# Kernel tuning notes

Hardware: AMD Instinct MI355X
Metric: run time of the kernel (lower is better)

Reference implementation:

```python
import jax, jax.numpy as jnp
import numpy as np

NEG_SLOPE = 0.2
BN_EPS = 1e-5
SM_EPS = 1e-16


def gatv2_conv(x, src, dst, num_nodes, Wl, bl, Wr, br, att, bias, concat):
    # x: [N, Fin]; att: [H, C]
    H, C = att.shape
    xl = (x @ Wl + bl).reshape(-1, H, C)  # source-side (x_j), lin_l
    xr = (x @ Wr + br).reshape(-1, H, C)  # target-side (x_i), lin_r
    e = jax.nn.leaky_relu(xl[src] + xr[dst], NEG_SLOPE)          # [E, H, C]
    logits = jnp.einsum('ehc,hc->eh', e, att)                    # [E, H]
    m = jax.ops.segment_max(logits, dst, num_segments=num_nodes)  # [N, H]
    expv = jnp.exp(logits - m[dst])
    denom = jax.ops.segment_sum(expv, dst, num_segments=num_nodes)
    alpha = expv / (denom[dst] + SM_EPS)                          # [E, H]
    msg = xl[src] * alpha[:, :, None]                             # [E, H, C]
    out = jax.ops.segment_sum(msg, dst, num_segments=num_nodes)   # [N, H, C]
    out = out.reshape(num_nodes, H * C) if concat else out.mean(axis=1)
    return out + bias


def batchnorm(x, gamma, beta):
    mean = x.mean(axis=0)
    var = x.var(axis=0)  # biased, as torch uses for normalization
    return gamma * (x - mean) * jax.lax.rsqrt(var + BN_EPS) + beta


def setup_inputs() -> dict:
    key = jax.random.key(0)
    ks = jax.random.split(key, 16)
    N, E = 50000, 800000
    Fin, Hid, Out, H = 128, 64, 64, 4
    s = 0.05
    inp = {
        'x': jax.random.normal(ks[0], (N, Fin), jnp.float32),
        'edge_index': jax.random.randint(ks[1], (2, E), 0, N, jnp.int64),
        # conv1 (heads=4, concat=False)
        'Wl1': jax.random.normal(ks[2], (Fin, H * Hid), jnp.float32) * s,
        'bl1': jnp.zeros((H * Hid,), jnp.float32),
        'Wr1': jax.random.normal(ks[3], (Fin, H * Hid), jnp.float32) * s,
        'br1': jnp.zeros((H * Hid,), jnp.float32),
        'att1': jax.random.normal(ks[4], (H, Hid), jnp.float32) * s,
        'bias1': jnp.zeros((Hid,), jnp.float32),
        'g1': jnp.ones((Hid,), jnp.float32),
        'beta1': jnp.zeros((Hid,), jnp.float32),
        # conv2 (heads=1, concat=True -> same as single head)
        'Wl2': jax.random.normal(ks[5], (Hid, Out), jnp.float32) * s,
        'bl2': jnp.zeros((Out,), jnp.float32),
        'Wr2': jax.random.normal(ks[6], (Hid, Out), jnp.float32) * s,
        'br2': jnp.zeros((Out,), jnp.float32),
        'att2': jax.random.normal(ks[7], (1, Out), jnp.float32) * s,
        'bias2': jnp.zeros((Out,), jnp.float32),
        'g2': jnp.ones((Out,), jnp.float32),
        'beta2': jnp.zeros((Out,), jnp.float32),
    }
    return inp


def reference(x, edge_index, Wl1, bl1, Wr1, br1, att1, bias1, g1, beta1,
              Wl2, bl2, Wr2, br2, att2, bias2, g2, beta2):
    N = x.shape[0]
    loops = jnp.arange(N, dtype=edge_index.dtype)  # PyG add_self_loops=True
    src = jnp.concatenate([edge_index[0], loops])
    dst = jnp.concatenate([edge_index[1], loops])
    h = gatv2_conv(x, src, dst, N, Wl1, bl1, Wr1, br1, att1, bias1, concat=False)
    h = jax.nn.relu(batchnorm(h, g1, beta1))  # dropout = identity (eval)
    h = gatv2_conv(h, src, dst, N, Wl2, bl2, Wr2, br2, att2, bias2, concat=True)
    h = jax.nn.relu(batchnorm(h, g2, beta2))
    return h
```

## Files before the change

### kernel.cpp

```cpp
#include <hip/hip_runtime.h>
#include <hip/hip_bf16.h>
#include <math.h>

#define TPB 256

typedef __attribute__((ext_vector_type(8))) _Float16 hfrag8;
typedef __attribute__((ext_vector_type(2))) _Float16 h2;
typedef __attribute__((ext_vector_type(4))) float f32x4;

union HU { unsigned int u; h2 h; };

static __device__ __forceinline__ h2 as_h2(unsigned int u) { HU c; c.u = u; return c.h; }
static __device__ __forceinline__ unsigned short f2h_bits(float f) {
  union { _Float16 h; unsigned short s; } c; c.h = (_Float16)f; return c.s;
}

#define DPP_ROR(v, C) __int_as_float(__builtin_amdgcn_update_dpp( \
    __float_as_int(v), __float_as_int(v), (C), 0xf, 0xf, false))
static __device__ __forceinline__ float red16(float p) {
  p += DPP_ROR(p, 0x121);
  p += DPP_ROR(p, 0x122);
  p += DPP_ROR(p, 0x124);
  p += DPP_ROR(p, 0x128);
  return p;
}

__global__ void k_deg_wprep(const int* __restrict__ ei, int E, int ET, int* __restrict__ deg,
                            const float* __restrict__ Wl1, const float* __restrict__ Wr1,
                            const float* __restrict__ Wl2, const float* __restrict__ Wr2,
                            unsigned short* __restrict__ wt1l, unsigned short* __restrict__ wt1r,
                            unsigned short* __restrict__ wt2l, unsigned short* __restrict__ wt2r,
                            int egrid) {
  int b = blockIdx.x;
  if (b < egrid) {
    int e = b * TPB + threadIdx.x;
    if (e < ET) {
      int dst = (e < E) ? ei[E + e] : (e - E);
      atomicAdd(&deg[dst], 1);
    }
    return;
  }
  int i = (b - egrid) * TPB + threadIdx.x;
  if (i < 32768) {
    int c = i >> 7, k = i & 127;
    wt1l[i] = f2h_bits(Wl1[(size_t)k * 256 + c]);
  } else if (i < 65536) {
    int j = i - 32768; int c = j >> 7, k = j & 127;
    wt1r[j] = f2h_bits(Wr1[(size_t)k * 256 + c]);
  } else if (i < 69632) {
    int j = i - 65536; int c = j >> 6, k = j & 63;
    wt2l[j] = f2h_bits(Wl2[(size_t)k * 64 + c]);
  } else if (i < 73728) {
    int j = i - 69632; int c = j >> 6, k = j & 63;
    wt2r[j] = f2h_bits(Wr2[(size_t)k * 64 + c]);
  }
}

__global__ void k_scanf(const int* __restrict__ deg, int N,
                        int* __restrict__ rowoff, int* __restrict__ cursor) {
  __shared__ int sm[TPB];
  int t = threadIdx.x;
  int pref = blockIdx.x * TPB;
  int acc = 0;
  for (int j = t; j < pref; j += TPB) acc += (deg[j] + 3) & ~3;
  sm[t] = acc;
  __syncthreads();
  for (int d = TPB / 2; d > 0; d >>= 1) {
    if (t < d) sm[t] += sm[t + d];
    __syncthreads();
  }
  int base = sm[0];
  __syncthreads();
  int i = pref + t;
  int v = (i < N) ? ((deg[i] + 3) & ~3) : 0;
  sm[t] = v;
  __syncthreads();
  for (int d = 1; d < TPB; d <<= 1) {
    int tmp = (t >= d) ? sm[t - d] : 0;
    __syncthreads();
    sm[t] += tmp;
    __syncthreads();
  }
  if (i < N) {
    int off = base + sm[t] - v;
    rowoff[i] = off;
    cursor[i] = off;
  }
}

__global__ void k_fill(const int* __restrict__ ei, int E, int ET,
                       int* __restrict__ cursor, int* __restrict__ csrc) {
  int e = blockIdx.x * blockDim.x + threadIdx.x;
  if (e >= ET) return;
  int src, dst;
  if (e < E) { src = ei[e]; dst = ei[E + e]; } else { src = dst = e - E; }
  int pos = atomicAdd(&cursor[dst], 1);
  csrc[pos] = src;
}

__global__ void k_gemm_mfma(const float* __restrict__ A, const float* __restrict__ affine,
                            const unsigned short* __restrict__ Wt0, const float* __restrict__ b0,
                            const unsigned short* __restrict__ Wt1, const float* __restrict__ b1,
                            unsigned short* __restrict__ out0, unsigned short* __restrict__ out1,
                            int M, int K, int Nc, int mtile, int nt4) {
  extern __shared__ short lds[];
  short* As = lds;
  short* Bls = lds + 64 * K;
  short* Brs = lds + 128 * K;
  int m, nt;
  if (nt4) {
    int xcd = blockIdx.x & 7, gg = blockIdx.x >> 3;
    nt = gg & 3; m = ((gg >> 2) << 3) | xcd;
    if (m >= mtile) return;
  } else {
    m = blockIdx.x; nt = 0;
  }
  const int r0 = m * 64, n0 = nt * 64;
  const int tid = threadIdx.x;
  const int Kb = K * 2;

  const int fpr = K >> 2;
  for (int idx = tid; idx < 64 * fpr; idx += TPB) {
    int row = idx / fpr, c4 = idx - row * fpr;
    int gr = r0 + row;
    float4 v = make_float4(0.f, 0.f, 0.f, 0.f);
    if (gr < M) v = *(const float4*)(A + (size_t)gr * K + c4 * 4);
    if (affine) {
      int c = c4 * 4;
      v.x = fmaxf(v.x * affine[c + 0] + affine[64 + c + 0], 0.f);
      v.y = fmaxf(v.y * affine[c + 1] + affine[64 + c + 1], 0.f);
      v.z = fmaxf(v.z * affine[c + 2] + affine[64 + c + 2], 0.f);
      v.w = fmaxf(v.w * affine[c + 3] + affine[64 + c + 3], 0.f);
    }
    ushort4 pk;
    pk.x = f2h_bits(v.x); pk.y = f2h_bits(v.y); pk.z = f2h_bits(v.z); pk.w = f2h_bits(v.w);
    int kb = (c4 * 8) ^ ((row & 7) << 4);
    *(ushort4*)((char*)As + row * Kb + kb) = pk;
  }
  const int cpr = K >> 3;
  for (int idx = tid; idx < 64 * cpr; idx += TPB) {
    int c = idx / cpr, k8 = (idx - c * cpr) * 8;
    int kb = (k8 * 2) ^ ((c & 7) << 4);
    uint4 w0 = *(const uint4*)(Wt0 + (size_t)(n0 + c) * K + k8);
    *(uint4*)((char*)Bls + c * Kb + kb) = w0;
    uint4 w1 = *(const uint4*)(Wt1 + (size_t)(n0 + c) * K + k8);
    *(uint4*)((char*)Brs + c * Kb + kb) = w1;
  }
  __syncthreads();

  const int w = tid >> 6, lane = tid & 63;
  const int arow = w * 16 + (lane & 15);
  const int l16 = (lane >> 4) << 3;
  f32x4 accL[4], accR[4];
#pragma unroll
  for (int i = 0; i < 4; ++i) { accL[i] = (f32x4)0.f; accR[i] = (f32x4)0.f; }
  for (int k0 = 0; k0 < K; k0 += 32) {
    int kb = (k0 + l16) * 2;
    hfrag8 af = *(hfrag8*)((char*)As + arow * Kb + (kb ^ ((arow & 7) << 4)));
#pragma unroll
    for (int cf = 0; cf < 4; ++cf) {
      int col = cf * 16 + (lane & 15);
      int cb = col * Kb + (kb ^ ((col & 7) << 4));
      hfrag8 bl = *(hfrag8*)((char*)Bls + cb);
      accL[cf] = __builtin_amdgcn_mfma_f32_16x16x32_f16(af, bl, accL[cf], 0, 0, 0);
      hfrag8 br = *(hfrag8*)((char*)Brs + cb);
      accR[cf] = __builtin_amdgcn_mfma_f32_16x16x32_f16(af, br, accR[cf], 0, 0, 0);
    }
  }
  const int rbase = r0 + w * 16 + ((lane >> 4) << 2);
  const int cbase = n0 + (lane & 15);
#pragma unroll
  for (int cf = 0; cf < 4; ++cf) {
    int gcol = cbase + cf * 16;
    float bb0 = b0[gcol], bb1 = b1[gcol];
#pragma unroll
    for (int r = 0; r < 4; ++r) {
      int grow = rbase + r;
      if (grow < M) {
        out0[(size_t)grow * Nc + gcol] = f2h_bits(accL[cf][r] + bb0);
        out1[(size_t)grow * Nc + gcol] = f2h_bits(accR[cf][r] + bb1);
      }
    }
  }
}

__global__ __launch_bounds__(TPB) void k_gat1(
    const unsigned short* __restrict__ xl, const unsigned short* __restrict__ xr,
    const int* __restrict__ rowoff, const int* __restrict__ deg,
    const int* __restrict__ csrc,
    const float* __restrict__ att, const float* __restrict__ bias,
    float* __restrict__ out, int N) {
  int node = (blockIdx.x * TPB + threadIdx.x) >> 6;
  int lane = threadIdx.x & 63;
  if (node >= N) return;
  int l4 = lane * 4;
  float4 atv = *(const float4*)(att + l4);
  h2 at01, at23;
  at01.x = (_Float16)atv.x; at01.y = (_Float16)atv.y;
  at23.x = (_Float16)atv.z; at23.y = (_Float16)atv.w;
  float4 bb = *(const float4*)(bias + l4);
  uint2 rv = *(const uint2*)(xr + (node << 8) + l4);
  h2 xr01 = as_h2(rv.x), xr23 = as_h2(rv.y);
  const _Float16 c02 = (_Float16)0.2f;
  int beg = rowoff[node];
  int dg = deg[node];
  int endR = beg + dg;
  int endF = beg + (dg & ~3);
  float s = 0.f, a0 = 0.f, a1 = 0.f, a2 = 0.f, a3 = 0.f;
  int k = beg;
  for (; k < endF; k += 4) {
    int4 q = *(const int4*)(csrc + k);
    uint2 vv[4];
    vv[0] = *(const uint2*)(xl + (q.x << 8) + l4);
    vv[1] = *(const uint2*)(xl + (q.y << 8) + l4);
    vv[2] = *(const uint2*)(xl + (q.z << 8) + l4);
    vv[3] = *(const uint2*)(xl + (q.w << 8) + l4);
    float ps[4];
#pragma unroll
    for (int u = 0; u < 4; ++u) {
      h2 x01 = as_h2(vv[u].x), x23 = as_h2(vv[u].y);
      h2 t01 = x01 + xr01, t23 = x23 + xr23;
      h2 l01 = __builtin_elementwise_max(t01, t01 * c02);
      h2 l23 = __builtin_elementwise_max(t23, t23 * c02);
      ps[u] = __builtin_amdgcn_fdot2(l01, at01,
              __builtin_amdgcn_fdot2(l23, at23, 0.f, false), false);
    }
#pragma unroll
    for (int u = 0; u < 4; ++u) ps[u] = red16(ps[u]);
#pragma unroll
    for (int u = 0; u < 4; ++u) {
      float wv = __expf(ps[u]);
      h2 x01 = as_h2(vv[u].x), x23 = as_h2(vv[u].y);
      s += wv;
      a0 += wv * (float)x01.x; a1 += wv * (float)x01.y;
      a2 += wv * (float)x23.x; a3 += wv * (float)x23.y;
    }
  }
  if (k < endR) {
    int4 q = *(const int4*)(csrc + k);
    uint2 vv[4];
    vv[0] = *(const uint2*)(xl + (q.x << 8) + l4);
    vv[1] = *(const uint2*)(xl + (q.y << 8) + l4);
    vv[2] = *(const uint2*)(xl + (q.z << 8) + l4);
    vv[3] = *(const uint2*)(xl + (q.w << 8) + l4);
    float ps[4];
#pragma unroll
    for (int u = 0; u < 4; ++u) {
      h2 x01 = as_h2(vv[u].x), x23 = as_h2(vv[u].y);
      h2 t01 = x01 + xr01, t23 = x23 + xr23;
      h2 l01 = __builtin_elementwise_max(t01, t01 * c02);
      h2 l23 = __builtin_elementwise_max(t23, t23 * c02);
      ps[u] = __builtin_amdgcn_fdot2(l01, at01,
              __builtin_amdgcn_fdot2(l23, at23, 0.f, false), false);
    }
#pragma unroll
    for (int u = 0; u < 4; ++u) ps[u] = red16(ps[u]);
#pragma unroll
    for (int u = 0; u < 4; ++u) {
      float wv = (k + u < endR) ? __expf(ps[u]) : 0.f;
      h2 x01 = as_h2(vv[u].x), x23 = as_h2(vv[u].y);
      s += wv;
      a0 += wv * (float)x01.x; a1 += wv * (float)x01.y;
      a2 += wv * (float)x23.x; a3 += wv * (float)x23.y;
    }
  }
  float inv = 1.f / (s + 1e-16f);
  a0 *= inv; a1 *= inv; a2 *= inv; a3 *= inv;
  a0 += __shfl_xor(a0, 16); a0 += __shfl_xor(a0, 32);
  a1 += __shfl_xor(a1, 16); a1 += __shfl_xor(a1, 32);
  a2 += __shfl_xor(a2, 16); a2 += __shfl_xor(a2, 32);
  a3 += __shfl_xor(a3, 16); a3 += __shfl_xor(a3, 32);
  if (lane < 16) {
    float4 o;
    o.x = a0 * 0.25f + bb.x;
    o.y = a1 * 0.25f + bb.y;
    o.z = a2 * 0.25f + bb.z;
    o.w = a3 * 0.25f + bb.w;
    *(float4*)(out + (node << 6) + l4) = o;
  }
}

__global__ __launch_bounds__(TPB) void k_gat2(
    const unsigned short* __restrict__ xl, const unsigned short* __restrict__ xr,
    const int* __restrict__ rowoff, const int* __restrict__ deg,
    const int* __restrict__ csrc,
    const float* __restrict__ att, const float* __restrict__ bias,
    float* __restrict__ out, int N) {
  int node = (blockIdx.x * TPB + threadIdx.x) >> 6;
  int lane = threadIdx.x & 63;
  if (node >= N) return;
  int grp = lane >> 4, c4 = (lane & 15) * 4;
  float4 atv = *(const float4*)(att + c4);
  h2 at01, at23;
  at01.x = (_Float16)atv.x; at01.y = (_Float16)atv.y;
  at23.x = (_Float16)atv.z; at23.y = (_Float16)atv.w;
  float4 bb = *(const float4*)(bias + c4);
  uint2 rv = *(const uint2*)(xr + (node << 6) + c4);
  h2 xr01 = as_h2(rv.x), xr23 = as_h2(rv.y);
  const _Float16 c02 = (_Float16)0.2f;
  int beg = rowoff[node];
  int dg = deg[node];
  int endR = beg + dg;
  int quads = (dg + 3) >> 2;
  float s = 0.f, a0 = 0.f, a1 = 0.f, a2 = 0.f, a3 = 0.f;
  for (int it = 0; it < quads; ++it) {
    int kk = beg + it * 4 + grp;
    int src = csrc[kk];
    bool ok = kk < endR;
    uint2 v = *(const uint2*)(xl + (src << 6) + c4);
    h2 x01 = as_h2(v.x), x23 = as_h2(v.y);
    h2 t01 = x01 + xr01, t23 = x23 + xr23;
    h2 l01 = __builtin_elementwise_max(t01, t01 * c02);
    h2 l23 = __builtin_elementwise_max(t23, t23 * c02);
    float p = __builtin_amdgcn_fdot2(l01, at01,
              __builtin_amdgcn_fdot2(l23, at23, 0.f, false), false);
    p = red16(p);
    float wv = ok ? __expf(p) : 0.f;
    s += wv;
    a0 += wv * (float)x01.x; a1 += wv * (float)x01.y;
    a2 += wv * (float)x23.x; a3 += wv * (float)x23.y;
  }
  s += __shfl_xor(s, 16); s += __shfl_xor(s, 32);
  a0 += __shfl_xor(a0, 16); a0 += __shfl_xor(a0, 32);
  a1 += __shfl_xor(a1, 16); a1 += __shfl_xor(a1, 32);
  a2 += __shfl_xor(a2, 16); a2 += __shfl_xor(a2, 32);
  a3 += __shfl_xor(a3, 16); a3 += __shfl_xor(a3, 32);
  if (lane < 16) {
    float inv = 1.f / (s + 1e-16f);
    float4 o;
    o.x = a0 * inv + bb.x;
    o.y = a1 * inv + bb.y;
    o.z = a2 * inv + bb.z;
    o.w = a3 * inv + bb.w;
    *(float4*)(out + (node << 6) + c4) = o;
  }
}

__global__ void k_bnstatfin(const float* __restrict__ in, int N, float* __restrict__ part,
                            int* __restrict__ counter, const float* __restrict__ g,
                            const float* __restrict__ beta, float* __restrict__ ab) {
  __shared__ float sm[TPB], sq[TPB];
  __shared__ float fin[TPB];
  __shared__ int lastsm;
  int col = threadIdx.x & 63;
  int rq = threadIdx.x >> 6;
  float s0 = 0.f, q0 = 0.f, s1 = 0.f, q1 = 0.f;
  int stride = gridDim.x * 4;
  int r = blockIdx.x * 4 + rq;
  for (; r + stride < N; r += 2 * stride) {
    float v0 = in[(size_t)r * 64 + col];
    float v1 = in[(size_t)(r + stride) * 64 + col];
    s0 += v0; q0 += v0 * v0;
    s1 += v1; q1 += v1 * v1;
  }
  if (r < N) {
    float v0 = in[(size_t)r * 64 + col];
    s0 += v0; q0 += v0 * v0;
  }
  sm[threadIdx.x] = s0 + s1; sq[threadIdx.x] = q0 + q1;
  __syncthreads();
  if (threadIdx.x < 128) {
    float v;
    if (threadIdx.x < 64) {
      v = sm[threadIdx.x] + sm[threadIdx.x + 64] + sm[threadIdx.x + 128] + sm[threadIdx.x + 192];
    } else {
      int c = threadIdx.x - 64;
      v = sq[c] + sq[c + 64] + sq[c + 128] + sq[c + 192];
    }
    part[(size_t)blockIdx.x * 128 + threadIdx.x] = v;
  }
  __threadfence();
  __syncthreads();
  if (threadIdx.x == 0) lastsm = atomicAdd(counter, 1);
  __syncthreads();
  if (lastsm != gridDim.x - 1) return;
  __threadfence();
  int t = threadIdx.x;
  int c = t & 127, gidx = t >> 7;
  int B = gridDim.x;
  float acc0 = 0.f, acc1 = 0.f, acc2 = 0.f, acc3 = 0.f;
  int b = gidx;
  for (; b + 6 < B; b += 8) {
    acc0 += part[(size_t)b * 128 + c];
    acc1 += part[(size_t)(b + 2) * 128 + c];
    acc2 += part[(size_t)(b + 4) * 128 + c];
    acc3 += part[(size_t)(b + 6) * 128 + c];
  }
  for (; b < B; b += 2) acc0 += part[(size_t)b * 128 + c];
  fin[t] = (acc0 + acc1) + (acc2 + acc3);
  __syncthreads();
  if (t < 64) {
    float ts = fin[t] + fin[t + 128];
    float tq = fin[t + 64] + fin[t + 192];
    float mean = ts / (float)N;
    float var = tq / (float)N - mean * mean;
    float a = g[t] * rsqrtf(var + 1e-5f);
    ab[t] = a;
    ab[64 + t] = beta[t] - mean * a;
  }
}

__global__ void k_bnapply(const float* __restrict__ in, const float* __restrict__ ab,
                          float* __restrict__ out, int total4) {
  int idx = blockIdx.x * blockDim.x + threadIdx.x;
  if (idx >= total4) return;
  float4 v = *(const float4*)(in + (size_t)idx * 4);
  int c0 = (idx & 15) * 4;
  v.x = fmaxf(v.x * ab[c0 + 0] + ab[64 + c0 + 0], 0.f);
  v.y = fmaxf(v.y * ab[c0 + 1] + ab[64 + c0 + 1], 0.f);
  v.z = fmaxf(v.z * ab[c0 + 2] + ab[64 + c0 + 2], 0.f);
  v.w = fmaxf(v.w * ab[c0 + 3] + ab[64 + c0 + 3], 0.f);
  *(float4*)(out + (size_t)idx * 4) = v;
}

extern "C" void kernel_launch(void* const* d_in, const int* in_sizes, int n_in,
                              void* d_out, int out_size, void* d_ws, size_t ws_size,
                              hipStream_t stream) {
  const float* x     = (const float*)d_in[0];
  const int*   ei    = (const int*)d_in[1];
  const float* Wl1   = (const float*)d_in[2];
  const float* bl1   = (const float*)d_in[3];
  const float* Wr1   = (const float*)d_in[4];
  const float* br1   = (const float*)d_in[5];
  const float* att1  = (const float*)d_in[6];
  const float* bias1 = (const float*)d_in[7];
  const float* g1    = (const float*)d_in[8];
  const float* be1   = (const float*)d_in[9];
  const float* Wl2   = (const float*)d_in[10];
  const float* bl2   = (const float*)d_in[11];
  const float* Wr2   = (const float*)d_in[12];
  const float* br2   = (const float*)d_in[13];
  const float* att2  = (const float*)d_in[14];
  const float* bias2 = (const float*)d_in[15];
  const float* g2    = (const float*)d_in[16];
  const float* be2   = (const float*)d_in[17];
  float* out = (float*)d_out;

  const int N  = in_sizes[0] / 128;
  const int E  = in_sizes[1] / 2;
  const int ET = E + N;
  const int ETP = ET + 4 * ((N + 255) & ~255);
  const int SB = (N + TPB - 1) / TPB;

  char* p = (char*)d_ws;
  auto take = [&](size_t b) { char* q = p; p += (b + 255) & ~(size_t)255; return q; };

  unsigned short* xl1 = (unsigned short*)take((size_t)N * 256 * 2);
  unsigned short* xr1 = (unsigned short*)take((size_t)N * 256 * 2);
  unsigned short* xl2 = (unsigned short*)take((size_t)N * 64 * 2);
  unsigned short* xr2 = (unsigned short*)take((size_t)N * 64 * 2);
  float* out1 = (float*)take((size_t)N * 64 * 4);
  unsigned short* wt1l = (unsigned short*)take(256 * 128 * 2);
  unsigned short* wt1r = (unsigned short*)take(256 * 128 * 2);
  unsigned short* wt2l = (unsigned short*)take(64 * 64 * 2);
  unsigned short* wt2r = (unsigned short*)take(64 * 64 * 2);
  int* deg    = (int*)take((size_t)N * 4);
  int* ctr    = (int*)take(512);
  int* csrc   = (int*)take((size_t)ETP * 4 + 16);
  size_t zero_bytes = (char*)(csrc + ETP) + 16 - (char*)deg;
  int* rowoff = (int*)take((size_t)(N + 1) * 4);
  int* cursor = (int*)take((size_t)N * 4);
  float* part = (float*)take((size_t)256 * 128 * 4);
  float* ab1  = (float*)take(128 * 4);
  float* ab2  = (float*)take(128 * 4);
  (void)ws_size; (void)n_in; (void)out_size;

  int egrid = (ET + TPB - 1) / TPB;
  int wgrid = (73728 + TPB - 1) / TPB;
  int ngrid = (N + 3) / 4;
  int mtile = (N + 63) / 64;
  int mg8 = (mtile + 7) / 8;
  int total4 = N * 16;

  hipMemsetAsync(deg, 0, zero_bytes, stream);
  k_deg_wprep<<<egrid + wgrid, TPB, 0, stream>>>(ei, E, ET, deg, Wl1, Wr1, Wl2, Wr2,
                                                 wt1l, wt1r, wt2l, wt2r, egrid);
  k_scanf<<<SB, TPB, 0, stream>>>(deg, N, rowoff, cursor);
  k_fill<<<egrid, TPB, 0, stream>>>(ei, E, ET, cursor, csrc);

  k_gemm_mfma<<<mg8 * 32, TPB, 3 * 64 * 128 * 2, stream>>>(
      x, nullptr, wt1l, bl1, wt1r, br1, xl1, xr1, N, 128, 256, mtile, 1);
  k_gat1<<<ngrid, TPB, 0, stream>>>(xl1, xr1, rowoff, deg, csrc, att1, bias1, out1, N);
  k_bnstatfin<<<256, TPB, 0, stream>>>(out1, N, part, ctr, g1, be1, ab1);

  k_gemm_mfma<<<mtile, TPB, 3 * 64 * 64 * 2, stream>>>(
      out1, ab1, wt2l, bl2, wt2r, br2, xl2, xr2, N, 64, 64, mtile, 0);
  k_gat2<<<ngrid, TPB, 0, stream>>>(xl2, xr2, rowoff, deg, csrc, att2, bias2, out, N);
  k_bnstatfin<<<256, TPB, 0, stream>>>(out, N, part, ctr + 64, g2, be2, ab2);
  k_bnapply<<<(total4 + TPB - 1) / TPB, TPB, 0, stream>>>(out, ab2, out, total4);
}
```

Measured before the change: 356.2 us.

## Shrink memset, store layer-1 output in fp16, enlarge GEMM row tile

Several changes at once. The memset no longer clears the whole CSR source array; k_fill zeroes only the padding slots past each node's degree. The layer-1 GAT output is stored as fp16 instead of fp32, and both the BN-stat kernel and the second GEMM read fp16. The MFMA GEMM now computes 128 rows per block, with two A fragments per wave reusing each B fragment. This cuts memset and intermediate traffic and improves weight reuse, at the cost of extra fp16 rounding before batchnorm and higher LDS and register use per block.

```diff
diff --git a/kernel.cpp b/kernel.cpp
--- a/kernel.cpp
+++ b/kernel.cpp
@@ -9,6 +9,7 @@
 typedef __attribute__((ext_vector_type(4))) float f32x4;
 
 union HU { unsigned int u; h2 h; };
+union US8 { unsigned short us[8]; uint4 v; };
 
 static __device__ __forceinline__ h2 as_h2(unsigned int u) { HU c; c.u = u; return c.h; }
 static __device__ __forceinline__ unsigned short f2h_bits(float f) {
@@ -88,25 +89,35 @@
   }
 }
 
-__global__ void k_fill(const int* __restrict__ ei, int E, int ET,
+__global__ void k_fill(const int* __restrict__ ei, int E, int ET, int N,
+                       const int* __restrict__ rowoff, const int* __restrict__ deg,
                        int* __restrict__ cursor, int* __restrict__ csrc) {
   int e = blockIdx.x * blockDim.x + threadIdx.x;
-  if (e >= ET) return;
-  int src, dst;
-  if (e < E) { src = ei[e]; dst = ei[E + e]; } else { src = dst = e - E; }
-  int pos = atomicAdd(&cursor[dst], 1);
-  csrc[pos] = src;
-}
-
-__global__ void k_gemm_mfma(const float* __restrict__ A, const float* __restrict__ affine,
+  if (e < ET) {
+    int src, dst;
+    if (e < E) { src = ei[e]; dst = ei[E + e]; } else { src = dst = e - E; }
+    csrc[atomicAdd(&cursor[dst], 1)] = src;
+  } else {
+    int i = e - ET;
+    if (i < N) {
+      int dg = deg[i];
+      int beg = rowoff[i] + dg;
+      int end = rowoff[i] + ((dg + 3) & ~3);
+      for (int k = beg; k < end; ++k) csrc[k] = 0;
+    }
+  }
+}
+
+__global__ void k_gemm_mfma(const void* __restrict__ Avoid, int af16,
+                            const float* __restrict__ affine,
                             const unsigned short* __restrict__ Wt0, const float* __restrict__ b0,
                             const unsigned short* __restrict__ Wt1, const float* __restrict__ b1,
                             unsigned short* __restrict__ out0, unsigned short* __restrict__ out1,
                             int M, int K, int Nc, int mtile, int nt4) {
   extern __shared__ short lds[];
   short* As = lds;
-  short* Bls = lds + 64 * K;
-  short* Brs = lds + 128 * K;
+  short* Bls = lds + 128 * K;
+  short* Brs = lds + 192 * K;
   int m, nt;
   if (nt4) {
     int xcd = blockIdx.x & 7, gg = blockIdx.x >> 3;
@@ -115,27 +126,45 @@
   } else {
     m = blockIdx.x; nt = 0;
   }
-  const int r0 = m * 64, n0 = nt * 64;
+  const int r0 = m * 128, n0 = nt * 64;
   const int tid = threadIdx.x;
   const int Kb = K * 2;
 
-  const int fpr = K >> 2;
-  for (int idx = tid; idx < 64 * fpr; idx += TPB) {
-    int row = idx / fpr, c4 = idx - row * fpr;
-    int gr = r0 + row;
-    float4 v = make_float4(0.f, 0.f, 0.f, 0.f);
-    if (gr < M) v = *(const float4*)(A + (size_t)gr * K + c4 * 4);
-    if (affine) {
-      int c = c4 * 4;
-      v.x = fmaxf(v.x * affine[c + 0] + affine[64 + c + 0], 0.f);
-      v.y = fmaxf(v.y * affine[c + 1] + affine[64 + c + 1], 0.f);
-      v.z = fmaxf(v.z * affine[c + 2] + affine[64 + c + 2], 0.f);
-      v.w = fmaxf(v.w * affine[c + 3] + affine[64 + c + 3], 0.f);
-    }
-    ushort4 pk;
-    pk.x = f2h_bits(v.x); pk.y = f2h_bits(v.y); pk.z = f2h_bits(v.z); pk.w = f2h_bits(v.w);
-    int kb = (c4 * 8) ^ ((row & 7) << 4);
-    *(ushort4*)((char*)As + row * Kb + kb) = pk;
+  if (af16) {
+    const unsigned short* A16 = (const unsigned short*)Avoid;
+    const int cpr8 = K >> 3;
+    for (int idx = tid; idx < 128 * cpr8; idx += TPB) {
+      int row = idx / cpr8, k8 = (idx - row * cpr8) * 8;
+      int gr = r0 + row;
+      uint4 av = make_uint4(0, 0, 0, 0);
+      if (gr < M) av = *(const uint4*)(A16 + (size_t)gr * K + k8);
+      unsigned int wds[4] = {av.x, av.y, av.z, av.w};
+      US8 res;
+#pragma unroll
+      for (int j = 0; j < 4; ++j) {
+        h2 hv = as_h2(wds[j]);
+        int c = k8 + j * 2;
+        float f0 = fmaxf((float)hv.x * affine[c] + affine[64 + c], 0.f);
+        float f1 = fmaxf((float)hv.y * affine[c + 1] + affine[64 + c + 1], 0.f);
+        res.us[j * 2] = f2h_bits(f0);
+        res.us[j * 2 + 1] = f2h_bits(f1);
+      }
+      int kb = (k8 * 2) ^ ((row & 7) << 4);
+      *(uint4*)((char*)As + row * Kb + kb) = res.v;
+    }
+  } else {
+    const float* A = (const float*)Avoid;
+    const int fpr = K >> 2;
+    for (int idx = tid; idx < 128 * fpr; idx += TPB) {
+      int row = idx / fpr, c4 = idx - row * fpr;
+      int gr = r0 + row;
+      float4 v = make_float4(0.f, 0.f, 0.f, 0.f);
+      if (gr < M) v = *(const float4*)(A + (size_t)gr * K + c4 * 4);
+      ushort4 pk;
+      pk.x = f2h_bits(v.x); pk.y = f2h_bits(v.y); pk.z = f2h_bits(v.z); pk.w = f2h_bits(v.w);
+      int kb = (c4 * 8) ^ ((row & 7) << 4);
+      *(ushort4*)((char*)As + row * Kb + kb) = pk;
+    }
   }
   const int cpr = K >> 3;
   for (int idx = tid; idx < 64 * cpr; idx += TPB) {
@@ -149,36 +178,45 @@
   __syncthreads();
 
   const int w = tid >> 6, lane = tid & 63;
-  const int arow = w * 16 + (lane & 15);
+  const int arow0 = w * 32 + (lane & 15);
+  const int arow1 = arow0 + 16;
   const int l16 = (lane >> 4) << 3;
-  f32x4 accL[4], accR[4];
-#pragma unroll
-  for (int i = 0; i < 4; ++i) { accL[i] = (f32x4)0.f; accR[i] = (f32x4)0.f; }
+  f32x4 accL[2][4], accR[2][4];
+#pragma unroll
+  for (int g = 0; g < 2; ++g)
+#pragma unroll
+    for (int i = 0; i < 4; ++i) { accL[g][i] = (f32x4)0.f; accR[g][i] = (f32x4)0.f; }
   for (int k0 = 0; k0 < K; k0 += 32) {
     int kb = (k0 + l16) * 2;
-    hfrag8 af = *(hfrag8*)((char*)As + arow * Kb + (kb ^ ((arow & 7) << 4)));
+    hfrag8 af0 = *(hfrag8*)((char*)As + arow0 * Kb + (kb ^ ((arow0 & 7) << 4)));
+    hfrag8 af1 = *(hfrag8*)((char*)As + arow1 * Kb + (kb ^ ((arow1 & 7) << 4)));
 #pragma unroll
     for (int cf = 0; cf < 4; ++cf) {
       int col = cf * 16 + (lane & 15);
       int cb = col * Kb + (kb ^ ((col & 7) << 4));
       hfrag8 bl = *(hfrag8*)((char*)Bls + cb);
-      accL[cf] = __builtin_amdgcn_mfma_f32_16x16x32_f16(af, bl, accL[cf], 0, 0, 0);
+      accL[0][cf] = __builtin_amdgcn_mfma_f32_16x16x32_f16(af0, bl, accL[0][cf], 0, 0, 0);
+      accL[1][cf] = __builtin_amdgcn_mfma_f32_16x16x32_f16(af1, bl, accL[1][cf], 0, 0, 0);
       hfrag8 br = *(hfrag8*)((char*)Brs + cb);
-      accR[cf] = __builtin_amdgcn_mfma_f32_16x16x32_f16(af, br, accR[cf], 0, 0, 0);
-    }
-  }
-  const int rbase = r0 + w * 16 + ((lane >> 4) << 2);
+      accR[0][cf] = __builtin_amdgcn_mfma_f32_16x16x32_f16(af0, br, accR[0][cf], 0, 0, 0);
+      accR[1][cf] = __builtin_amdgcn_mfma_f32_16x16x32_f16(af1, br, accR[1][cf], 0, 0, 0);
+    }
+  }
   const int cbase = n0 + (lane & 15);
 #pragma unroll
-  for (int cf = 0; cf < 4; ++cf) {
-    int gcol = cbase + cf * 16;
-    float bb0 = b0[gcol], bb1 = b1[gcol];
-#pragma unroll
-    for (int r = 0; r < 4; ++r) {
-      int grow = rbase + r;
-      if (grow < M) {
-        out0[(size_t)grow * Nc + gcol] = f2h_bits(accL[cf][r] + bb0);
-        out1[(size_t)grow * Nc + gcol] = f2h_bits(accR[cf][r] + bb1);
+  for (int g = 0; g < 2; ++g) {
+    const int rbase = r0 + w * 32 + g * 16 + ((lane >> 4) << 2);
+#pragma unroll
+    for (int cf = 0; cf < 4; ++cf) {
+      int gcol = cbase + cf * 16;
+      float bb0 = b0[gcol], bb1 = b1[gcol];
+#pragma unroll
+      for (int r = 0; r < 4; ++r) {
+        int grow = rbase + r;
+        if (grow < M) {
+          out0[(size_t)grow * Nc + gcol] = f2h_bits(accL[g][cf][r] + bb0);
+          out1[(size_t)grow * Nc + gcol] = f2h_bits(accR[g][cf][r] + bb1);
+        }
       }
     }
   }
@@ -189,7 +227,7 @@
     const int* __restrict__ rowoff, const int* __restrict__ deg,
     const int* __restrict__ csrc,
     const float* __restrict__ att, const float* __restrict__ bias,
-    float* __restrict__ out, int N) {
+    unsigned short* __restrict__ out, int N) {
   int node = (blockIdx.x * TPB + threadIdx.x) >> 6;
   int lane = threadIdx.x & 63;
   if (node >= N) return;
@@ -271,12 +309,12 @@
   a2 += __shfl_xor(a2, 16); a2 += __shfl_xor(a2, 32);
   a3 += __shfl_xor(a3, 16); a3 += __shfl_xor(a3, 32);
   if (lane < 16) {
-    float4 o;
-    o.x = a0 * 0.25f + bb.x;
-    o.y = a1 * 0.25f + bb.y;
-    o.z = a2 * 0.25f + bb.z;
-    o.w = a3 * 0.25f + bb.w;
-    *(float4*)(out + (node << 6) + l4) = o;
+    ushort4 o;
+    o.x = f2h_bits(a0 * 0.25f + bb.x);
+    o.y = f2h_bits(a1 * 0.25f + bb.y);
+    o.z = f2h_bits(a2 * 0.25f + bb.z);
+    o.w = f2h_bits(a3 * 0.25f + bb.w);
+    *(ushort4*)(out + (node << 6) + l4) = o;
   }
 }
 
@@ -336,25 +374,29 @@
   }
 }
 
-__global__ void k_bnstatfin(const float* __restrict__ in, int N, float* __restrict__ part,
-                            int* __restrict__ counter, const float* __restrict__ g,
-                            const float* __restrict__ beta, float* __restrict__ ab) {
+__global__ void k_bnstatfin(const void* __restrict__ inv_, int f16in, int N,
+                            float* __restrict__ part, int* __restrict__ counter,
+                            const float* __restrict__ g, const float* __restrict__ beta,
+                            float* __restrict__ ab) {
   __shared__ float sm[TPB], sq[TPB];
   __shared__ float fin[TPB];
   __shared__ int lastsm;
+  const float* inf = (const float*)inv_;
+  const _Float16* inh = (const _Float16*)inv_;
   int col = threadIdx.x & 63;
   int rq = threadIdx.x >> 6;
   float s0 = 0.f, q0 = 0.f, s1 = 0.f, q1 = 0.f;
   int stride = gridDim.x * 4;
   int r = blockIdx.x * 4 + rq;
   for (; r + stride < N; r += 2 * stride) {
-    float v0 = in[(size_t)r * 64 + col];
-    float v1 = in[(size_t)(r + stride) * 64 + col];
+    float v0 = f16in ? (float)inh[(size_t)r * 64 + col] : inf[(size_t)r * 64 + col];
+    float v1 = f16in ? (float)inh[(size_t)(r + stride) * 64 + col]
+                     : inf[(size_t)(r + stride) * 64 + col];
     s0 += v0; q0 += v0 * v0;
     s1 += v1; q1 += v1 * v1;
   }
   if (r < N) {
-    float v0 = in[(size_t)r * 64 + col];
+    float v0 = f16in ? (float)inh[(size_t)r * 64 + col] : inf[(size_t)r * 64 + col];
     s0 += v0; q0 += v0 * v0;
   }
   sm[threadIdx.x] = s0 + s1; sq[threadIdx.x] = q0 + q1;
@@ -449,15 +491,15 @@
   unsigned short* xr1 = (unsigned short*)take((size_t)N * 256 * 2);
   unsigned short* xl2 = (unsigned short*)take((size_t)N * 64 * 2);
   unsigned short* xr2 = (unsigned short*)take((size_t)N * 64 * 2);
-  float* out1 = (float*)take((size_t)N * 64 * 4);
+  unsigned short* out1 = (unsigned short*)take((size_t)N * 64 * 2);
   unsigned short* wt1l = (unsigned short*)take(256 * 128 * 2);
   unsigned short* wt1r = (unsigned short*)take(256 * 128 * 2);
   unsigned short* wt2l = (unsigned short*)take(64 * 64 * 2);
   unsigned short* wt2r = (unsigned short*)take(64 * 64 * 2);
   int* deg    = (int*)take((size_t)N * 4);
   int* ctr    = (int*)take(512);
+  size_t zero_bytes = (char*)ctr + 512 - (char*)deg;
   int* csrc   = (int*)take((size_t)ETP * 4 + 16);
-  size_t zero_bytes = (char*)(csrc + ETP) + 16 - (char*)deg;
   int* rowoff = (int*)take((size_t)(N + 1) * 4);
   int* cursor = (int*)take((size_t)N * 4);
   float* part = (float*)take((size_t)256 * 128 * 4);
@@ -467,25 +509,26 @@
 
   int egrid = (ET + TPB - 1) / TPB;
   int wgrid = (73728 + TPB - 1) / TPB;
+  int fgrid = (ET + N + TPB - 1) / TPB;
   int ngrid = (N + 3) / 4;
-  int mtile = (N + 63) / 64;
-  int mg8 = (mtile + 7) / 8;
+  int mt128 = (N + 127) / 128;
+  int mg8 = (mt128 + 7) / 8;
   int total4 = N * 16;
 
   hipMemsetAsync(deg, 0, zero_bytes, stream);
   k_deg_wprep<<<egrid + wgrid, TPB, 0, stream>>>(ei, E, ET, deg, Wl1, Wr1, Wl2, Wr2,
                                                  wt1l, wt1r, wt2l, wt2r, egrid);
   k_scanf<<<SB, TPB, 0, stream>>>(deg, N, rowoff, cursor);
-  k_fill<<<egrid, TPB, 0, stream>>>(ei, E, ET, cursor, csrc);
-
-  k_gemm_mfma<<<mg8 * 32, TPB, 3 * 64 * 128 * 2, stream>>>(
-      x, nullptr, wt1l, bl1, wt1r, br1, xl1, xr1, N, 128, 256, mtile, 1);
+  k_fill<<<fgrid, TPB, 0, stream>>>(ei, E, ET, N, rowoff, deg, cursor, csrc);
+
+  k_gemm_mfma<<<mg8 * 32, TPB, (128 + 64 + 64) * 128 * 2, stream>>>(
+      x, 0, nullptr, wt1l, bl1, wt1r, br1, xl1, xr1, N, 128, 256, mt128, 1);
   k_gat1<<<ngrid, TPB, 0, stream>>>(xl1, xr1, rowoff, deg, csrc, att1, bias1, out1, N);
-  k_bnstatfin<<<256, TPB, 0, stream>>>(out1, N, part, ctr, g1, be1, ab1);
-
-  k_gemm_mfma<<<mtile, TPB, 3 * 64 * 64 * 2, stream>>>(
-      out1, ab1, wt2l, bl2, wt2r, br2, xl2, xr2, N, 64, 64, mtile, 0);
+  k_bnstatfin<<<256, TPB, 0, stream>>>(out1, 1, N, part, ctr, g1, be1, ab1);
+
+  k_gemm_mfma<<<mt128, TPB, (128 + 64 + 64) * 64 * 2, stream>>>(
+      out1, 1, ab1, wt2l, bl2, wt2r, br2, xl2, xr2, N, 64, 64, mt128, 0);
   k_gat2<<<ngrid, TPB, 0, stream>>>(xl2, xr2, rowoff, deg, csrc, att2, bias2, out, N);
-  k_bnstatfin<<<256, TPB, 0, stream>>>(out, N, part, ctr + 64, g2, be2, ab2);
+  k_bnstatfin<<<256, TPB, 0, stream>>>(out, 0, N, part, ctr + 64, g2, be2, ab2);
   k_bnapply<<<(total4 + TPB - 1) / TPB, TPB, 0, stream>>>(out, ab2, out, total4);
 }
```

Measured after the change: 375.9 us. 1.06x slower.
